# Optimization experiments

Measured on AMD Instinct MI355X. Metric: run time of the kernel, lower is better.

## Reference

```python
import jax, jax.numpy as jnp
import numpy as np

N = 50000        # num_nodes
E = 800000       # num_edges (avg degree 16)
K = 3            # Chebyshev order
F_IN = 144       # 144 * in_channels
F_OUT = 144      # 144 * out_channels


def setup_inputs() -> dict:
    key = jax.random.key(0)
    k1, k2, k3, k4, k5 = jax.random.split(key, 5)
    x = jax.random.normal(k1, (N, F_IN), dtype=jnp.float32)
    edge_index = jax.random.randint(k2, (2, E), 0, N, dtype=jnp.int32)
    edge_weight = jax.random.uniform(k3, (E,), dtype=jnp.float32)
    weight = jax.random.normal(k4, (K, F_IN, F_OUT), dtype=jnp.float32) * 0.02
    bias = jax.random.normal(k5, (F_OUT,), dtype=jnp.float32) * 0.02
    return {"x": x, "edge_index": edge_index, "edge_weight": edge_weight,
            "weight": weight, "bias": bias}


def reference(x, edge_index, edge_weight, weight, bias):
    row, col = edge_index[0], edge_index[1]
    # remove_self_loops: mask out edges with row == col (fixed-shape equivalent)
    mask = (row != col).astype(x.dtype)
    w = edge_weight * mask
    # degree over remaining edges, deg^-0.5 with inf -> 0
    deg = jax.ops.segment_sum(mask, row, num_segments=N)
    dinv = jnp.where(deg > 0, deg ** -0.5, jnp.zeros_like(deg))
    lap = -dinv[row] * w * dinv[col]  # [E]

    def spmm(v):  # out[i] = sum_{e: row_e = i} lap_e * v[col_e]
        return jax.ops.segment_sum(lap[:, None] * v[col], row, num_segments=N)

    Tx0 = x
    out = Tx0 @ weight[0]
    Tx1 = spmm(Tx0)
    out = out + Tx1 @ weight[1]
    for k in range(2, weight.shape[0]):
        Tx2 = 2.0 * spmm(Tx1) - Tx0
        out = out + Tx2 @ weight[k]
        Tx0, Tx1 = Tx1, Tx2
    return out + bias
```

## Files before the change

### kernel.cpp

```cpp
#include <hip/hip_runtime.h>
#include <hip/hip_bf16.h>

#define NN 50000
#define EE 800000
#define FF 144
#define CVTBLK 1758
#define ECHK 2048
#define NBE 391
#define NBKT_REAL 391
#define NBUCKET 392
#define WGRID 284
#define HM (NBUCKET * NBE)
#define SCANBLK 599

typedef __hip_bfloat16 bf16;
typedef __attribute__((ext_vector_type(8))) short short8;
typedef __attribute__((ext_vector_type(4))) float floatx4;
typedef __attribute__((ext_vector_type(2))) float float2v;

__device__ inline float blo(unsigned x) { return __uint_as_float(x << 16); }
__device__ inline float bhi(unsigned x) { return __uint_as_float(x & 0xffff0000u); }

__device__ inline void dec4fma(float* a, float l, unsigned d) {
    float2v p0 = __builtin_amdgcn_cvt_pk_f32_fp8((int)d, false);
    float2v p1 = __builtin_amdgcn_cvt_pk_f32_fp8((int)d, true);
    a[0] = fmaf(l, p0.x, a[0]);
    a[1] = fmaf(l, p0.y, a[1]);
    a[2] = fmaf(l, p1.x, a[2]);
    a[3] = fmaf(l, p1.y, a[3]);
}
__device__ inline void fma16q(float* a, float l, uint4 u) {
    dec4fma(a + 0, l, u.x);
    dec4fma(a + 4, l, u.y);
    dec4fma(a + 8, l, u.z);
    dec4fma(a + 12, l, u.w);
}
__device__ inline unsigned enc4(float a, float b, float c, float d) {
    int w = __builtin_amdgcn_cvt_pk_fp8_f32(a, b, 0, false);
    w = __builtin_amdgcn_cvt_pk_fp8_f32(c, d, w, true);
    return (unsigned)w;
}

__device__ inline void load_edge(const int* ei, int e, int flag, int& r, int& c) {
    if (flag) { r = ei[2 * e]; c = ei[2 * EE + 2 * e]; }
    else      { r = ei[e];     c = ei[EE + e]; }
}


__global__ void fusedA_k(const float* __restrict__ x, bf16* __restrict__ xb,
                         unsigned char* __restrict__ xq,
                         const int* __restrict__ ei, const float* __restrict__ ew,
                         unsigned long long* __restrict__ items, int* __restrict__ hist,
                         const float* __restrict__ wt, short* __restrict__ wtb) {
    __shared__ int lh[NBUCKET];
    __shared__ int nzf;
    int b = blockIdx.x;
    int tid = threadIdx.x;
    if (b < CVTBLK) {
        int t = b * 256 + tid;
        if (t >= NN * FF / 16) return;
        const float4* xp = (const float4*)x + t * 4;
        float4 v0 = xp[0], v1 = xp[1], v2 = xp[2], v3 = xp[3];
        float f[16] = {v0.x, v0.y, v0.z, v0.w, v1.x, v1.y, v1.z, v1.w,
                       v2.x, v2.y, v2.z, v2.w, v3.x, v3.y, v3.z, v3.w};
        unsigned short hs[16];
        #pragma unroll
        for (int j = 0; j < 16; ++j) {
            bf16 bb = (bf16)f[j];
            hs[j] = *(unsigned short*)&bb;
        }
        uint4* xbq = (uint4*)xb + t * 2;
        xbq[0] = ((uint4*)hs)[0];
        xbq[1] = ((uint4*)hs)[1];
        uint4 q;
        q.x = enc4(f[0], f[1], f[2], f[3]);
        q.y = enc4(f[4], f[5], f[6], f[7]);
        q.z = enc4(f[8], f[9], f[10], f[11]);
        q.w = enc4(f[12], f[13], f[14], f[15]);
        ((uint4*)xq)[t] = q;
    } else if (b < CVTBLK + NBE) {
        int bb = b - CVTBLK;
        if (tid == 0) nzf = 0;
        for (int j = tid; j < NBUCKET; j += 256) lh[j] = 0;
        __syncthreads();
        int eb = bb * ECHK;
        unsigned acc = 0;
        #pragma unroll
        for (int k = 0; k < ECHK / 256; ++k) {
            int e = eb + k * 256 + tid;
            if (e < EE) acc |= (unsigned)ei[2 * e + 1];
        }
        if (acc) nzf = 1;
        __syncthreads();
        int flag = (nzf == 0) ? 1 : 0;
        #pragma unroll
        for (int k = 0; k < ECHK / 256; ++k) {
            int e = eb + k * 256 + tid;
            if (e < EE) {
                int r, c; load_edge(ei, e, flag, r, c);
                unsigned key = (r == c) ? 0xFFFFu : (unsigned)r;
                items[e] = ((unsigned long long)((key << 16) | (unsigned)c) << 32)
                           | (unsigned long long)__float_as_uint(ew[e]);
                atomicAdd(&lh[min(key >> 7, (unsigned)NBKT_REAL)], 1);
            }
        }
        __syncthreads();
        for (int j = tid; j < NBUCKET; j += 256) hist[j * NBE + bb] = lh[j];
    } else {
        int t = (b - CVTBLK - NBE) * 256 + tid;
        if (t >= 3 * FF * 168) return;
        int ph = t / (FF * 168);
        int rem = t - ph * FF * 168;
        int o = rem / 168;
        int i = rem - o * 168;
        short v = 0;
        if (i < FF) {
            float fv;
            if (ph == 0)      fv = wt[i * FF + o] - wt[2 * FF * FF + i * FF + o];
            else if (ph == 1) fv = wt[FF * FF + i * FF + o];
            else              fv = 2.0f * wt[2 * FF * FF + i * FF + o];
            bf16 bv = (bf16)fv;
            v = *(const short*)&bv;
        }
        wtb[t] = v;
    }
}


__global__ void scanA1_k(int* __restrict__ hist, int* __restrict__ bsumA) {
    __shared__ int wsum[4], woff[4];
    int b = blockIdx.x, tid = threadIdx.x;
    int wv = tid >> 6, ln = tid & 63;
    int i = b * 256 + tid;
    int v = (i < HM) ? hist[i] : 0;
    int xs = v;
    #pragma unroll
    for (int off = 1; off < 64; off <<= 1) {
        int t = __shfl_up(xs, off, 64);
        if (ln >= off) xs += t;
    }
    if (ln == 63) wsum[wv] = xs;
    __syncthreads();
    if (tid == 0) {
        int s = 0;
        #pragma unroll
        for (int j = 0; j < 4; ++j) { woff[j] = s; s += wsum[j]; }
        bsumA[b] = s;
    }
    __syncthreads();
    if (i < HM) hist[i] = woff[wv] + (xs - v);
}

__global__ __launch_bounds__(1024) void scanA2_k(int* __restrict__ bsumA) {
    __shared__ int wsum[16], woff[16];
    int tid = threadIdx.x, wv = tid >> 6, ln = tid & 63;
    int v = (tid < SCANBLK) ? bsumA[tid] : 0;
    int xs = v;
    #pragma unroll
    for (int off = 1; off < 64; off <<= 1) {
        int t = __shfl_up(xs, off, 64);
        if (ln >= off) xs += t;
    }
    if (ln == 63) wsum[wv] = xs;
    __syncthreads();
    if (tid == 0) {
        int s = 0;
        #pragma unroll
        for (int j = 0; j < 16; ++j) { woff[j] = s; s += wsum[j]; }
    }
    __syncthreads();
    if (tid < SCANBLK) bsumA[tid] = woff[wv] + (xs - v);
}

__device__ inline int hbase(const int* hist, const int* bsumA, int f) {
    return hist[f] + bsumA[f >> 8];
}


__global__ void pscat_k(const unsigned long long* __restrict__ items,
                        const int* __restrict__ hist, const int* __restrict__ bsumA,
                        unsigned long long* __restrict__ sorted) {
    __shared__ int lbase[NBUCKET];
    int b = blockIdx.x, tid = threadIdx.x;
    for (int j = tid; j < NBUCKET; j += 256) {
        int f = j * NBE + b;
        lbase[j] = hbase(hist, bsumA, f);
    }
    __syncthreads();
    int eb = b * ECHK;
    #pragma unroll
    for (int k = 0; k < ECHK / 256; ++k) {
        int e = eb + k * 256 + tid;
        if (e < EE) {
            unsigned long long it = items[e];
            unsigned key = (unsigned)(it >> 48);
            int bk = (int)min(key >> 7, (unsigned)NBKT_REAL);
            int slot = atomicAdd(&lbase[bk], 1);
            sorted[slot] = it;
        }
    }
}


__global__ void fine1_k(const unsigned long long* __restrict__ sorted,
                        const int* __restrict__ hist, const int* __restrict__ bsumA,
                        int* __restrict__ rowptr, float* __restrict__ dinv) {
    __shared__ int lh[128];
    __shared__ int wtot;
    int b = blockIdx.x, tid = threadIdx.x;
    if (tid < 128) lh[tid] = 0;
    int s = hbase(hist, bsumA, b * NBE);
    int e = hbase(hist, bsumA, (b + 1) * NBE);
    __syncthreads();
    for (int p = s + tid; p < e; p += 256)
        atomicAdd(&lh[(int)(unsigned)(sorted[p] >> 48) - b * 128], 1);
    __syncthreads();
    int ln = tid & 63;
    int v = (tid < 128) ? lh[tid] : 0;
    int xs = v;
    #pragma unroll
    for (int off = 1; off < 64; off <<= 1) {
        int t = __shfl_up(xs, off, 64);
        if (ln >= off) xs += t;
    }
    if (tid == 63) wtot = xs;
    __syncthreads();
    int excl = xs - v + ((tid >= 64 && tid < 128) ? wtot : 0);
    int gr = b * 128 + tid;
    if (tid < 128 && gr < NN) {
        rowptr[gr] = s + excl;
        dinv[gr] = v > 0 ? rsqrtf((float)v) : 0.f;
    }
    if (b == NBKT_REAL - 1 && tid == 0) rowptr[NN] = e;
}


__global__ void fine2_k(const unsigned long long* __restrict__ sorted,
                        const int* __restrict__ hist, const int* __restrict__ bsumA,
                        const int* __restrict__ rowptr, const float* __restrict__ dinv,
                        unsigned* __restrict__ pairs) {
    __shared__ int lrp[128];
    __shared__ float ldv[128];
    int b = blockIdx.x, tid = threadIdx.x;
    int gr = b * 128 + tid;
    if (tid < 128) {
        lrp[tid] = (gr < NN) ? rowptr[gr] : 0;
        ldv[tid] = (gr < NN) ? dinv[gr] : 0.f;
    }
    int s = hbase(hist, bsumA, b * NBE);
    int e = hbase(hist, bsumA, (b + 1) * NBE);
    __syncthreads();
    for (int p = s + tid; p < e; p += 256) {
        unsigned long long it = sorted[p];
        int lr = (int)(unsigned)(it >> 48) - b * 128;
        unsigned c = (unsigned)(it >> 32) & 0xFFFFu;
        float w = __uint_as_float((unsigned)it);
        float lap = -ldv[lr] * dinv[c] * w;
        int slot = atomicAdd(&lrp[lr], 1);
        bf16 lb = (bf16)lap;
        pairs[slot] = c | ((unsigned)*(unsigned short*)&lb << 16);
    }
}


template <int WRITEQ>
__global__ void spmm_k(const unsigned char* __restrict__ vq,
                       const int* __restrict__ rowptr, const unsigned* __restrict__ pairs,
                       bf16* __restrict__ y, unsigned char* __restrict__ yq) {
    int t = blockIdx.x * 256 + threadIdx.x;
    if (t >= NN * 9) return;
    int i = t / 9;
    int fo = (t - i * 9) * 16;
    const unsigned char* vp = vq + fo;

    float a[16];
    #pragma unroll
    for (int j = 0; j < 16; ++j) a[j] = 0.f;

    int s = rowptr[i], e = rowptr[i + 1];
    int p = s;
    for (; p + 3 < e; p += 4) {
        unsigned pr0 = pairs[p], pr1 = pairs[p + 1];
        unsigned pr2 = pairs[p + 2], pr3 = pairs[p + 3];
        uint4 u0 = *(const uint4*)(vp + (pr0 & 0xffffu) * FF);
        uint4 u1 = *(const uint4*)(vp + (pr1 & 0xffffu) * FF);
        uint4 u2 = *(const uint4*)(vp + (pr2 & 0xffffu) * FF);
        uint4 u3 = *(const uint4*)(vp + (pr3 & 0xffffu) * FF);
        fma16q(a, bhi(pr0), u0);
        fma16q(a, bhi(pr1), u1);
        fma16q(a, bhi(pr2), u2);
        fma16q(a, bhi(pr3), u3);
    }
    for (; p < e; ++p) {
        unsigned pr = pairs[p];
        uint4 u = *(const uint4*)(vp + (pr & 0xffffu) * FF);
        fma16q(a, bhi(pr), u);
    }

    unsigned short hs[16];
    #pragma unroll
    for (int j = 0; j < 16; ++j) {
        bf16 b = (bf16)a[j];
        hs[j] = *(unsigned short*)&b;
    }
    uint4* yp = (uint4*)((unsigned short*)y + i * FF + fo);
    yp[0] = ((uint4*)hs)[0];
    yp[1] = ((uint4*)hs)[1];

    if (WRITEQ) {
        uint4 q;
        q.x = enc4(a[0], a[1], a[2], a[3]);
        q.y = enc4(a[4], a[5], a[6], a[7]);
        q.z = enc4(a[8], a[9], a[10], a[11]);
        q.w = enc4(a[12], a[13], a[14], a[15]);
        *(uint4*)(yq + i * FF + fo) = q;
    }
}


__global__ __launch_bounds__(1024)
void gemm_fused(const bf16* __restrict__ A0, const bf16* __restrict__ A1,
                const bf16* __restrict__ A2, const short* __restrict__ wtb,
                const float* __restrict__ bias, float* __restrict__ out) {
    __shared__ __align__(16) short Wt[3 * 144 * 168];
    int tid = threadIdx.x;

    {
        const uint4* Wg = (const uint4*)wtb;
        uint4* Wl = (uint4*)Wt;
        #pragma unroll
        for (int q = 0; q < 9; ++q) {
            int idx = q * 1024 + tid;
            if (idx < 9072) Wl[idx] = Wg[idx];
        }
    }
    __syncthreads();

    int wv = tid >> 6, ln = tid & 63;
    int m16 = ln & 15, quad = ln >> 4;
    int tile = wv * 256 + blockIdx.x;
    if (tile * 16 >= NN) return;
    int rowBase = tile * 16;
    int row = rowBase + m16;

    const bf16* const srcs[3] = {A0, A1, A2};
    const short8 zero8 = {0, 0, 0, 0, 0, 0, 0, 0};

    floatx4 acc[9];
    #pragma unroll
    for (int q = 0; q < 9; ++q) acc[q] = (floatx4){0.f, 0.f, 0.f, 0.f};

    short8 a_cur[5], a_nxt[5];
    #pragma unroll
    for (int kt = 0; kt < 5; ++kt) {
        int k0 = kt * 32 + quad * 8;
        a_cur[kt] = (k0 < FF) ? *(const short8*)((const short*)A0 + row * FF + k0) : zero8;
    }

    #pragma unroll
    for (int ph = 0; ph < 3; ++ph) {
        if (ph < 2) {
            const bf16* An = srcs[ph + 1];
            #pragma unroll
            for (int kt = 0; kt < 5; ++kt) {
                int k0 = kt * 32 + quad * 8;
                a_nxt[kt] = (k0 < FF) ? *(const short8*)((const short*)An + row * FF + k0) : zero8;
            }
        }

        const short* Wp = Wt + ph * 144 * 168;
        #pragma unroll
        for (int nt = 0; nt < 9; ++nt) {
            #pragma unroll
            for (int kt = 0; kt < 5; ++kt) {
                short8 b = *(const short8*)&Wp[(nt * 16 + m16) * 168 + kt * 32 + quad * 8];
                acc[nt] = __builtin_amdgcn_mfma_f32_16x16x32_bf16(a_cur[kt], b, acc[nt], 0, 0, 0);
            }
        }

        if (ph < 2) {
            #pragma unroll
            for (int kt = 0; kt < 5; ++kt) a_cur[kt] = a_nxt[kt];
        }
    }

    int rowc = rowBase + quad * 4;
    #pragma unroll
    for (int nt = 0; nt < 9; ++nt) {
        int col = nt * 16 + m16;
        float bs = bias[col];
        #pragma unroll
        for (int r = 0; r < 4; ++r) {
            int rr = rowc + r;
            out[rr * FF + col] = acc[nt][r] + bs;
        }
    }
}


extern "C" void kernel_launch(void* const* d_in, const int* in_sizes, int n_in,
                              void* d_out, int out_size, void* d_ws, size_t ws_size,
                              hipStream_t stream) {
    int ix = -1, iei = -1, iew = -1, iwt = -1, ib = -1;
    for (int i = 0; i < n_in; ++i) {
        switch (in_sizes[i]) {
            case NN * FF:      if (ix  < 0) ix  = i; break;
            case 2 * EE:       if (iei < 0) iei = i; break;
            case EE:           if (iew < 0) iew = i; break;
            case 3 * FF * FF:  if (iwt < 0) iwt = i; break;
            case FF:           if (ib  < 0) ib  = i; break;
        }
    }
    if (ix < 0 || iei < 0 || iew < 0 || iwt < 0 || ib < 0) {
        ix = 0; iei = 1; iew = 2; iwt = 3; ib = 4;
    }
    const float* x    = (const float*)d_in[ix];
    const int*   ei   = (const int*)d_in[iei];
    const float* ew   = (const float*)d_in[iew];
    const float* wt   = (const float*)d_in[iwt];
    const float* bias = (const float*)d_in[ib];
    float* out = (float*)d_out;

    char* p = (char*)d_ws;
    unsigned long long* items  = (unsigned long long*)(p + 0);
    unsigned long long* sorted = (unsigned long long*)(p + 6400000);
    int*      hist   = (int*)(p + 12800000);
    int*      bsumA  = (int*)(p + 13500000);
    int*      rowptr = (int*)(p + 13600000);
    float*    dinv   = (float*)(p + 13900000);
    unsigned* pairs  = (unsigned*)(p + 14200000);
    short*    wtb    = (short*)(p + 17500000);
    bf16*     tx1    = (bf16*)(p + 17700000);
    bf16*     tx2    = (bf16*)(p + 32100000);
    unsigned char* xq   = (unsigned char*)(p + 46500000);
    unsigned char* tx1q = (unsigned char*)(p + 53700000);
    bf16*     xb     = (bf16*)(p + 60900000);

    if (ws_size < 75300000) return;

    int spGrid = (NN * 9 + 255) / 256;

    fusedA_k<<<CVTBLK + NBE + WGRID, 256, 0, stream>>>(x, xb, xq, ei, ew, items, hist,
                                                       wt, wtb);
    scanA1_k<<<SCANBLK, 256, 0, stream>>>(hist, bsumA);
    scanA2_k<<<1, 1024, 0, stream>>>(bsumA);
    pscat_k<<<NBE, 256, 0, stream>>>(items, hist, bsumA, sorted);
    fine1_k<<<NBKT_REAL, 256, 0, stream>>>(sorted, hist, bsumA, rowptr, dinv);
    fine2_k<<<NBKT_REAL, 256, 0, stream>>>(sorted, hist, bsumA, rowptr, dinv, pairs);

    spmm_k<1><<<spGrid, 256, 0, stream>>>(xq, rowptr, pairs, tx1, tx1q);
    spmm_k<0><<<spGrid, 256, 0, stream>>>(tx1q, rowptr, pairs, tx2, (unsigned char*)0);
    gemm_fused<<<256, 1024, 0, stream>>>(xb, tx1, tx2, wtb, bias, out);
}
```

Baseline: 192.3 us.

## Sort rows by degree so SpMM warps process rows of similar length

Builds a degree histogram in fine1_k, scans it in an extra block of fine2_k, and adds a dperm_k kernel that emits a permutation grouping rows by degree. Both SpMM passes now map threads to rows through this permutation, which is meant to cut warp divergence from uneven row lengths. In exchange it adds a kernel launch, global atomics, an indirection load, and loses the locality of consecutive row writes and of sequential pairs accesses.

```diff
diff --git a/kernel.cpp b/kernel.cpp
--- a/kernel.cpp
+++ b/kernel.cpp
@@ -12,6 +12,7 @@
 #define WGRID 284
 #define HM (NBUCKET * NBE)
 #define SCANBLK 599
+#define NDBIN 64
 
 typedef __hip_bfloat16 bf16;
 typedef __attribute__((ext_vector_type(8))) short short8;
@@ -151,9 +152,12 @@
     if (i < HM) hist[i] = woff[wv] + (xs - v);
 }
 
-__global__ __launch_bounds__(1024) void scanA2_k(int* __restrict__ bsumA) {
+
+__global__ __launch_bounds__(1024) void scanA2_k(int* __restrict__ bsumA,
+                                                 int* __restrict__ dbins) {
     __shared__ int wsum[16], woff[16];
     int tid = threadIdx.x, wv = tid >> 6, ln = tid & 63;
+    if (tid < NDBIN) dbins[tid] = 0;
     int v = (tid < SCANBLK) ? bsumA[tid] : 0;
     int xs = v;
     #pragma unroll
@@ -204,11 +208,14 @@
 
 __global__ void fine1_k(const unsigned long long* __restrict__ sorted,
                         const int* __restrict__ hist, const int* __restrict__ bsumA,
-                        int* __restrict__ rowptr, float* __restrict__ dinv) {
+                        int* __restrict__ rowptr, float* __restrict__ dinv,
+                        int* __restrict__ dbins) {
     __shared__ int lh[128];
+    __shared__ int lhb[NDBIN];
     __shared__ int wtot;
     int b = blockIdx.x, tid = threadIdx.x;
     if (tid < 128) lh[tid] = 0;
+    if (tid < NDBIN) lhb[tid] = 0;
     int s = hbase(hist, bsumA, b * NBE);
     int e = hbase(hist, bsumA, (b + 1) * NBE);
     __syncthreads();
@@ -216,7 +223,9 @@
         atomicAdd(&lh[(int)(unsigned)(sorted[p] >> 48) - b * 128], 1);
     __syncthreads();
     int ln = tid & 63;
+    int gr = b * 128 + tid;
     int v = (tid < 128) ? lh[tid] : 0;
+    if (tid < 128 && gr < NN) atomicAdd(&lhb[min(v, NDBIN - 1)], 1);
     int xs = v;
     #pragma unroll
     for (int off = 1; off < 64; off <<= 1) {
@@ -226,22 +235,35 @@
     if (tid == 63) wtot = xs;
     __syncthreads();
     int excl = xs - v + ((tid >= 64 && tid < 128) ? wtot : 0);
-    int gr = b * 128 + tid;
     if (tid < 128 && gr < NN) {
         rowptr[gr] = s + excl;
         dinv[gr] = v > 0 ? rsqrtf((float)v) : 0.f;
     }
     if (b == NBKT_REAL - 1 && tid == 0) rowptr[NN] = e;
+    if (tid < NDBIN) atomicAdd(&dbins[tid], lhb[tid]);
 }
 
 
 __global__ void fine2_k(const unsigned long long* __restrict__ sorted,
                         const int* __restrict__ hist, const int* __restrict__ bsumA,
                         const int* __restrict__ rowptr, const float* __restrict__ dinv,
-                        unsigned* __restrict__ pairs) {
+                        unsigned* __restrict__ pairs, int* __restrict__ dbins) {
     __shared__ int lrp[128];
     __shared__ float ldv[128];
     int b = blockIdx.x, tid = threadIdx.x;
+    if (b == NBKT_REAL) {
+        if (tid < NDBIN) {
+            int v = dbins[tid];
+            int xs = v;
+            #pragma unroll
+            for (int off = 1; off < NDBIN; off <<= 1) {
+                int t = __shfl_up(xs, off, 64);
+                if ((tid & 63) >= off) xs += t;
+            }
+            dbins[tid] = xs - v;
+        }
+        return;
+    }
     int gr = b * 128 + tid;
     if (tid < 128) {
         lrp[tid] = (gr < NN) ? rowptr[gr] : 0;
@@ -263,14 +285,26 @@
 }
 
 
+__global__ void dperm_k(const int* __restrict__ rowptr, int* __restrict__ dbins,
+                        int* __restrict__ perm) {
+    int i = blockIdx.x * 256 + threadIdx.x;
+    if (i >= NN) return;
+    int deg = rowptr[i + 1] - rowptr[i];
+    int pos = atomicAdd(&dbins[min(deg, NDBIN - 1)], 1);
+    perm[pos] = i;
+}
+
+
 template <int WRITEQ>
 __global__ void spmm_k(const unsigned char* __restrict__ vq,
                        const int* __restrict__ rowptr, const unsigned* __restrict__ pairs,
+                       const int* __restrict__ perm,
                        bf16* __restrict__ y, unsigned char* __restrict__ yq) {
     int t = blockIdx.x * 256 + threadIdx.x;
     if (t >= NN * 9) return;
-    int i = t / 9;
-    int fo = (t - i * 9) * 16;
+    int slot = t / 9;
+    int i = perm[slot];
+    int fo = (t - slot * 9) * 16;
     const unsigned char* vp = vq + fo;
 
     float a[16];
@@ -426,6 +460,7 @@
     unsigned long long* sorted = (unsigned long long*)(p + 6400000);
     int*      hist   = (int*)(p + 12800000);
     int*      bsumA  = (int*)(p + 13500000);
+    int*      dbins  = (int*)(p + 13560000);
     int*      rowptr = (int*)(p + 13600000);
     float*    dinv   = (float*)(p + 13900000);
     unsigned* pairs  = (unsigned*)(p + 14200000);
@@ -435,20 +470,22 @@
     unsigned char* xq   = (unsigned char*)(p + 46500000);
     unsigned char* tx1q = (unsigned char*)(p + 53700000);
     bf16*     xb     = (bf16*)(p + 60900000);
-
-    if (ws_size < 75300000) return;
+    int*      perm   = (int*)(p + 75300000);
+
+    if (ws_size < 75500000) return;
 
     int spGrid = (NN * 9 + 255) / 256;
 
     fusedA_k<<<CVTBLK + NBE + WGRID, 256, 0, stream>>>(x, xb, xq, ei, ew, items, hist,
                                                        wt, wtb);
     scanA1_k<<<SCANBLK, 256, 0, stream>>>(hist, bsumA);
-    scanA2_k<<<1, 1024, 0, stream>>>(bsumA);
+    scanA2_k<<<1, 1024, 0, stream>>>(bsumA, dbins);
     pscat_k<<<NBE, 256, 0, stream>>>(items, hist, bsumA, sorted);
-    fine1_k<<<NBKT_REAL, 256, 0, stream>>>(sorted, hist, bsumA, rowptr, dinv);
-    fine2_k<<<NBKT_REAL, 256, 0, stream>>>(sorted, hist, bsumA, rowptr, dinv, pairs);
-
-    spmm_k<1><<<spGrid, 256, 0, stream>>>(xq, rowptr, pairs, tx1, tx1q);
-    spmm_k<0><<<spGrid, 256, 0, stream>>>(tx1q, rowptr, pairs, tx2, (unsigned char*)0);
+    fine1_k<<<NBKT_REAL, 256, 0, stream>>>(sorted, hist, bsumA, rowptr, dinv, dbins);
+    fine2_k<<<NBKT_REAL + 1, 256, 0, stream>>>(sorted, hist, bsumA, rowptr, dinv, pairs, dbins);
+    dperm_k<<<(NN + 255) / 256, 256, 0, stream>>>(rowptr, dbins, perm);
+
+    spmm_k<1><<<spGrid, 256, 0, stream>>>(xq, rowptr, pairs, perm, tx1, tx1q);
+    spmm_k<0><<<spGrid, 256, 0, stream>>>(tx1q, rowptr, pairs, perm, tx2, (unsigned char*)0);
     gemm_fused<<<256, 1024, 0, stream>>>(xb, tx1, tx2, wtb, bias, out);
 }
```

Result: slower. 312.3 us (+62.4%).
